# Kernel tuning notes

Hardware: AMD Instinct MI355X
Metric: run time of the kernel (lower is better)

Reference implementation:

```python
import jax, jax.numpy as jnp
import numpy as np

N_QUBITS = 10
N_QLAYERS = 2
EMBED = 1024
B, S = 16, 1024
DIM = 2 ** N_QUBITS


def _apply_rx(state, theta, w, n):
    # state: [N, 2^n] complex; RX(theta) on wire w (wire 0 = most significant bit)
    nb = state.shape[0]
    left, right = 2 ** w, 2 ** (n - 1 - w)
    psi = state.reshape(nb, left, 2, right)
    t = jnp.asarray(theta, jnp.float32) * 0.5
    c, s = jnp.cos(t), jnp.sin(t)
    if c.ndim == 1:  # per-sample angles
        c, s = c[:, None, None], s[:, None, None]
    a0, a1 = psi[:, :, 0, :], psi[:, :, 1, :]
    n0 = c * a0 - 1j * s * a1
    n1 = -1j * s * a0 + c * a1
    return jnp.stack([n0, n1], axis=2).reshape(nb, -1)


def _apply_cnot(state, c, t, n):
    # CNOT with control wire c, target wire t
    psi = state.reshape((-1,) + (2,) * n)
    ctrl_ax, tgt_ax = c + 1, t + 1
    psi0, psi1 = jnp.split(psi, 2, axis=ctrl_ax)
    psi1 = jnp.flip(psi1, axis=tgt_ax)
    return jnp.concatenate([psi0, psi1], axis=ctrl_ax).reshape(state.shape)


def setup_inputs() -> dict:
    key = jax.random.key(0)
    ks = jax.random.split(key, 6)
    s1 = 1.0 / np.sqrt(EMBED)
    s2 = 1.0 / np.sqrt(N_QUBITS)
    return {
        "x": jax.random.normal(ks[0], (B, S, EMBED), jnp.float32),
        "W1": jax.random.uniform(ks[1], (N_QUBITS, EMBED), jnp.float32, -s1, s1),
        "b1": jax.random.uniform(ks[2], (N_QUBITS,), jnp.float32, -s1, s1),
        "qweights": jax.random.uniform(ks[3], (N_QLAYERS, N_QUBITS), jnp.float32, 0.0, 2.0 * np.pi),
        "W2": jax.random.uniform(ks[4], (EMBED, N_QUBITS), jnp.float32, -s2, s2),
        "b2": jax.random.uniform(ks[5], (EMBED,), jnp.float32, -s2, s2),
    }


def reference(x, W1, b1, qweights, W2, b2):
    n = N_QUBITS
    # linear_1
    ang = (jnp.einsum('bse,qe->bsq', x, W1) + b1).reshape(-1, n)  # [N, n]
    N = ang.shape[0]
    # |0...0> batched state vector
    state = jnp.zeros((N, DIM), jnp.complex64).at[:, 0].set(1.0)
    # AngleEmbedding: RX(ang[:, w]) on each wire
    for w in range(n):
        state = _apply_rx(state, ang[:, w], w, n)
    # BasicEntanglerLayers: RX rotations + CNOT ring per layer
    for l in range(N_QLAYERS):
        for w in range(n):
            state = _apply_rx(state, qweights[l, w], w, n)
        if n == 2:
            state = _apply_cnot(state, 0, 1, n)
        elif n > 2:
            for i in range(n):
                state = _apply_cnot(state, i, (i + 1) % n, n)
    # <Z_w> = sum_idx probs[idx] * (1 - 2*bit_w(idx))
    probs = jnp.real(state * jnp.conj(state))  # [N, 2^n]
    idx = jnp.arange(DIM)
    bits = (idx[:, None] >> (n - 1 - jnp.arange(n))[None, :]) & 1
    signs = (1 - 2 * bits).astype(jnp.float32)  # [2^n, n]
    ev = (probs @ signs).reshape(x.shape[0], x.shape[1], n)  # [B, S, n]
    # linear_2
    return jnp.einsum('bsq,eq->bse', ev, W2) + b2
```

## Files before the change

### kernel.cpp

```cpp
#include <hip/hip_runtime.h>

#define NQ 10
#define EMBED 1024
#define ROWS_PER_BLOCK 32
#define BLOCK 512


constexpr int kPop(int x) { int c = 0; for (int i = 0; i < 10; ++i) c += (x >> i) & 1; return c; }

constexpr int sigma_map(int a) {
    int b = 0;
    for (int i = 0; i < 9; ++i) b |= (((a >> i) & 1) ^ ((a >> (i + 1)) & 1)) << i;
    b |= (((a >> 9) & 1) ^ ((a >> 0) & 1) ^ ((a >> 1) & 1)) << 9;
    return b;
}

#define MAXT 40
struct Terms {
    int nt[NQ];
    int vm[NQ];
    int um[NQ];
    unsigned short tm[NQ][MAXT];
    unsigned short sm[NQ][MAXT];
    float sg[NQ][MAXT];
};

constexpr Terms gen_terms() {
    Terms t{};
    int inv_e[NQ] = {};
    for (int a = 0; a < 1024; ++a) {
        const int s = sigma_map(a);
        for (int q = 0; q < NQ; ++q) if (s == (1 << q)) inv_e[q] = a;
    }
    for (int q = 0; q < NQ; ++q) {
        const int u = inv_e[q];
        int v = 0;
        for (int w = 0; w < NQ; ++w) if ((u >> w) & 1) v ^= inv_e[w];
        t.um[q] = u; t.vm[q] = v;
        int n = 0;
        int S = 0;
        while (true) {
            int T = (((S >> 0) ^ (S >> 9)) & 1)
                  | ((((S >> 0) ^ (S >> 1) ^ (S >> 9)) & 1) << 1);
            for (int j = 2; j < 10; ++j) T |= ((((S >> (j - 1)) ^ (S >> j)) & 1) << j);
            if ((T & ~v) == 0) {
                const int p = kPop(T) + kPop(S);
                if (!(p & 1)) {
                    t.tm[q][n] = (unsigned short)T;
                    t.sm[q][n] = (unsigned short)S;
                    t.sg[q][n] = (p & 2) ? -1.f : 1.f;
                    ++n;
                }
            }
            if (S == u) break;
            S = (S - u) & u;
        }
        t.nt[q] = n;
    }
    return t;
}

constexpr Terms TT = gen_terms();

template <int CTRL, int RM>
__device__ __forceinline__ float dppadd(float v) {
    const int s = __builtin_amdgcn_update_dpp(0, __float_as_int(v), CTRL, RM, 0xF, true);
    return v + __int_as_float(s);
}
__device__ __forceinline__ float red32(float v) {
    v = dppadd<0xB1,  0xF>(v);
    v = dppadd<0x4E,  0xF>(v);
    v = dppadd<0x141, 0xF>(v);
    v = dppadd<0x140, 0xF>(v);
    v = dppadd<0x142, 0xA>(v);
    return v;
}

#define FMA1(ACC, XV, WW)                 \
    ACC = fmaf((XV).x, (WW).x, ACC);      \
    ACC = fmaf((XV).y, (WW).y, ACC);      \
    ACC = fmaf((XV).z, (WW).z, ACC);      \
    ACC = fmaf((XV).w, (WW).w, ACC);

extern "C" __global__ __launch_bounds__(BLOCK, 4)
void ffq_kernel(const float* __restrict__ x, const float* __restrict__ W1,
                const float* __restrict__ b1, const float* __restrict__ qw,
                const float* __restrict__ W2, const float* __restrict__ b2,
                float* __restrict__ out)
{
    __shared__ float sW1[NQ * EMBED];
    __shared__ float sCA[ROWS_PER_BLOCK][11];
    __shared__ float sSA[ROWS_PER_BLOCK][11];
    __shared__ float sEVv[ROWS_PER_BLOCK][11];

    const int tid  = threadIdx.x;
    const int lane = tid & 63;
    const int wv   = tid >> 6;
    const int o    = lane & 31;
    const int g    = lane >> 5;
    const int block0 = blockIdx.x * ROWS_PER_BLOCK;

    {
        const float4* src = (const float4*)W1;
        float4* dst = (float4*)sW1;
        #pragma unroll
        for (int i = 0; i < 5; ++i) dst[tid + BLOCK * i] = src[tid + BLOCK * i];
    }
    __syncthreads();

    {
        const int rloc0 = wv * 4 + g * 2;
        const float4* xr0 = (const float4*)(x + (size_t)(block0 + rloc0) * EMBED);
        const float4* xr1 = (const float4*)(x + (size_t)(block0 + rloc0 + 1) * EMBED);
        const float4* w1v = (const float4*)sW1;

        float4 xv0[4], xv1[4];
        #pragma unroll
        for (int k = 0; k < 4; ++k) { xv0[k] = xr0[k * 32 + o]; xv1[k] = xr1[k * 32 + o]; }

        float acc0[NQ], acc1[NQ];
        #pragma unroll
        for (int q = 0; q < NQ; ++q) { acc0[q] = 0.f; acc1[q] = 0.f; }

        float4 wA[5], wB[5], wC[5];

        #define HLOAD(BUF, H) {                                                  \
            _Pragma("unroll")                                                    \
            for (int q = 0; q < 5; ++q)                                          \
                BUF[q] = w1v[(((H) & 1) * 5 + q) * 256 + ((H) >> 1) * 32 + o];   \
        }
        #define HFMA(BUF, H) {                                                   \
            _Pragma("unroll")                                                    \
            for (int q = 0; q < 5; ++q) {                                        \
                FMA1(acc0[((H) & 1) * 5 + q], xv0[((H) >> 1) & 3], BUF[q]);      \
                FMA1(acc1[((H) & 1) * 5 + q], xv1[((H) >> 1) & 3], BUF[q]);      \
            }                                                                    \
        }
        #define XREFILL(K) {                                                     \
            xv0[(K) & 3] = xr0[((K) + 4) * 32 + o];                              \
            xv1[(K) & 3] = xr1[((K) + 4) * 32 + o];                              \
        }

        HLOAD(wA, 0);
        HLOAD(wB, 1);
        HLOAD(wC, 2);  HFMA(wA, 0);
        HLOAD(wA, 3);  HFMA(wB, 1);  XREFILL(0);
        HLOAD(wB, 4);  HFMA(wC, 2);
        HLOAD(wC, 5);  HFMA(wA, 3);  XREFILL(1);
        HLOAD(wA, 6);  HFMA(wB, 4);
        HLOAD(wB, 7);  HFMA(wC, 5);  XREFILL(2);
        HLOAD(wC, 8);  HFMA(wA, 6);
        HLOAD(wA, 9);  HFMA(wB, 7);  XREFILL(3);
        HLOAD(wB, 10); HFMA(wC, 8);
        HLOAD(wC, 11); HFMA(wA, 9);
        HLOAD(wA, 12); HFMA(wB, 10);
        HLOAD(wB, 13); HFMA(wC, 11);
        HLOAD(wC, 14); HFMA(wA, 12);
        HLOAD(wA, 15); HFMA(wB, 13);
                       HFMA(wC, 14);
                       HFMA(wA, 15);
        #undef HLOAD
        #undef HFMA
        #undef XREFILL

        #pragma unroll
        for (int q = 0; q < NQ; ++q) {
            acc0[q] = red32(acc0[q]);
            acc1[q] = red32(acc1[q]);
        }

        if (o == 16) {
            #pragma unroll
            for (int w = 0; w < NQ; ++w) {
                const float A = acc0[w] + b1[w] + qw[w];
                sCA[rloc0][w] = __cosf(A);
                sSA[rloc0][w] = __sinf(A);
            }
        } else if (o == 17) {
            #pragma unroll
            for (int w = 0; w < NQ; ++w) {
                const float A = acc1[w] + b1[w] + qw[w];
                sCA[rloc0 + 1][w] = __cosf(A);
                sSA[rloc0 + 1][w] = __sinf(A);
            }
        }
    }

    const int e4 = tid & 255;
    float w2f[40];
    {
        const float4* w2v = (const float4*)(W2 + e4 * 40);
        #pragma unroll
        for (int i = 0; i < 10; ++i) {
            float4 v = w2v[i];
            w2f[4*i+0] = v.x; w2f[4*i+1] = v.y; w2f[4*i+2] = v.z; w2f[4*i+3] = v.w;
        }
    }
    const float4 b2v = ((const float4*)b2)[e4];

    __syncthreads();

    if (lane < ROWS_PER_BLOCK) {
        const int row = lane;
        float ca[NQ], sa[NQ], cb[NQ], sb[NQ];
        #pragma unroll
        for (int w = 0; w < NQ; ++w) {
            ca[w] = sCA[row][w];
            sa[w] = sSA[row][w];
            const float B = qw[NQ + w];
            cb[w] = __cosf(B); sb[w] = __sinf(B);
        }
        #define EVQ(QC) do {                                                      \
            float ev = 0.f;                                                       \
            _Pragma("unroll")                                                     \
            for (int k = 0; k < TT.nt[QC]; ++k) {                                 \
                float P = TT.sg[QC][k];                                           \
                _Pragma("unroll")                                                 \
                for (int w = 0; w < NQ; ++w) {                                    \
                    if ((TT.vm[QC] >> w) & 1) P *= ((TT.tm[QC][k] >> w) & 1) ? sa[w] : ca[w]; \
                    if ((TT.um[QC] >> w) & 1) P *= ((TT.sm[QC][k] >> w) & 1) ? sb[w] : cb[w]; \
                }                                                                 \
                ev += P;                                                          \
            }                                                                     \
            sEVv[row][QC] = ev;                                                   \
        } while (0)
        switch (wv) {
            case 0: EVQ(0); break;
            case 1: EVQ(9); break;
            case 2: EVQ(7); break;
            case 3: EVQ(8); break;
            case 4: EVQ(5); EVQ(6); break;
            case 5: EVQ(3); EVQ(4); break;
            case 6: EVQ(1); EVQ(2); break;
            default: break;
        }
        #undef EVQ
    }

    __syncthreads();

    const int r0 = (tid >> 8) * 16;
    #pragma unroll
    for (int r = 0; r < 16; ++r) {
        const int rr = r0 + r;
        float evr[NQ];
        #pragma unroll
        for (int q = 0; q < NQ; ++q) evr[q] = sEVv[rr][q];
        float o0 = b2v.x, o1 = b2v.y, o2 = b2v.z, o3 = b2v.w;
        #pragma unroll
        for (int q = 0; q < NQ; ++q) {
            o0 = fmaf(evr[q], w2f[ 0 + q], o0);
            o1 = fmaf(evr[q], w2f[10 + q], o1);
            o2 = fmaf(evr[q], w2f[20 + q], o2);
            o3 = fmaf(evr[q], w2f[30 + q], o3);
        }
        float4 ov = {o0, o1, o2, o3};
        ((float4*)(out + (size_t)(block0 + rr) * EMBED))[e4] = ov;
    }
}

extern "C" void kernel_launch(void* const* d_in, const int* in_sizes, int n_in,
                              void* d_out, int out_size, void* d_ws, size_t ws_size,
                              hipStream_t stream) {
    (void)in_sizes; (void)n_in; (void)d_ws; (void)ws_size; (void)out_size;
    const float* x  = (const float*)d_in[0];
    const float* W1 = (const float*)d_in[1];
    const float* b1 = (const float*)d_in[2];
    const float* qw = (const float*)d_in[3];
    const float* W2 = (const float*)d_in[4];
    const float* b2 = (const float*)d_in[5];
    float* out = (float*)d_out;

    const int total_rows = 16 * 1024;
    dim3 grid(total_rows / ROWS_PER_BLOCK);
    ffq_kernel<<<grid, BLOCK, 0, stream>>>(x, W1, b1, qw, W2, b2, out);
}
```

Before: 28.35 us.

## Split fused kernel into expectation-value kernel and output projection kernel

Splits the single fused kernel into two launches. The first computes the per-row quantum expectation values and stashes them in the first ten floats of each output row. The second reads them back and runs the linear_2 projection on smaller 256-thread blocks of 8 rows each. The intent is to decouple the register-heavy expectation phase from the store-bound output phase and give the write stage more parallelism, at the cost of an extra launch and an extra global round trip for the expectation values.

New measurement: 36.06 us. 27.2% more time.

```diff
diff --git a/kernel.cpp b/kernel.cpp
--- a/kernel.cpp
+++ b/kernel.cpp
@@ -83,15 +83,13 @@
     ACC = fmaf((XV).w, (WW).w, ACC);
 
 extern "C" __global__ __launch_bounds__(BLOCK, 4)
-void ffq_kernel(const float* __restrict__ x, const float* __restrict__ W1,
-                const float* __restrict__ b1, const float* __restrict__ qw,
-                const float* __restrict__ W2, const float* __restrict__ b2,
-                float* __restrict__ out)
+void ffq_ev_kernel(const float* __restrict__ x, const float* __restrict__ W1,
+                   const float* __restrict__ b1, const float* __restrict__ qw,
+                   float* __restrict__ out)
 {
     __shared__ float sW1[NQ * EMBED];
     __shared__ float sCA[ROWS_PER_BLOCK][11];
     __shared__ float sSA[ROWS_PER_BLOCK][11];
-    __shared__ float sEVv[ROWS_PER_BLOCK][11];
 
     const int tid  = threadIdx.x;
     const int lane = tid & 63;
@@ -186,18 +184,6 @@
         }
     }
 
-    const int e4 = tid & 255;
-    float w2f[40];
-    {
-        const float4* w2v = (const float4*)(W2 + e4 * 40);
-        #pragma unroll
-        for (int i = 0; i < 10; ++i) {
-            float4 v = w2v[i];
-            w2f[4*i+0] = v.x; w2f[4*i+1] = v.y; w2f[4*i+2] = v.z; w2f[4*i+3] = v.w;
-        }
-    }
-    const float4 b2v = ((const float4*)b2)[e4];
-
     __syncthreads();
 
     if (lane < ROWS_PER_BLOCK) {
@@ -210,6 +196,7 @@
             const float B = qw[NQ + w];
             cb[w] = __cosf(B); sb[w] = __sinf(B);
         }
+        float* orow = out + (size_t)(block0 + row) * EMBED;
         #define EVQ(QC) do {                                                      \
             float ev = 0.f;                                                       \
             _Pragma("unroll")                                                     \
@@ -222,7 +209,7 @@
                 }                                                                 \
                 ev += P;                                                          \
             }                                                                     \
-            sEVv[row][QC] = ev;                                                   \
+            orow[QC] = ev;                                                        \
         } while (0)
         switch (wv) {
             case 0: EVQ(0); break;
@@ -236,26 +223,48 @@
         }
         #undef EVQ
     }
-
+}
+
+extern "C" __global__ __launch_bounds__(256, 4)
+void ffq_out_kernel(const float* __restrict__ W2, const float* __restrict__ b2,
+                    float* __restrict__ out)
+{
+    __shared__ float sev[80];
+
+    const int tid = threadIdx.x;
+    const int r0  = blockIdx.x * 8;
+
+    float w2f[40];
+    {
+        const float4* w2v = (const float4*)(W2 + tid * 40);
+        #pragma unroll
+        for (int i = 0; i < 10; ++i) {
+            float4 v = w2v[i];
+            w2f[4*i+0] = v.x; w2f[4*i+1] = v.y; w2f[4*i+2] = v.z; w2f[4*i+3] = v.w;
+        }
+    }
+    const float4 b2v = ((const float4*)b2)[tid];
+
+    if (tid < 80) {
+        const int rr = tid / 10;
+        const int qq = tid - rr * 10;
+        sev[tid] = out[(size_t)(r0 + rr) * EMBED + qq];
+    }
     __syncthreads();
 
-    const int r0 = (tid >> 8) * 16;
     #pragma unroll
-    for (int r = 0; r < 16; ++r) {
-        const int rr = r0 + r;
-        float evr[NQ];
-        #pragma unroll
-        for (int q = 0; q < NQ; ++q) evr[q] = sEVv[rr][q];
+    for (int rr = 0; rr < 8; ++rr) {
         float o0 = b2v.x, o1 = b2v.y, o2 = b2v.z, o3 = b2v.w;
         #pragma unroll
         for (int q = 0; q < NQ; ++q) {
-            o0 = fmaf(evr[q], w2f[ 0 + q], o0);
-            o1 = fmaf(evr[q], w2f[10 + q], o1);
-            o2 = fmaf(evr[q], w2f[20 + q], o2);
-            o3 = fmaf(evr[q], w2f[30 + q], o3);
+            const float e = sev[rr * 10 + q];
+            o0 = fmaf(e, w2f[ 0 + q], o0);
+            o1 = fmaf(e, w2f[10 + q], o1);
+            o2 = fmaf(e, w2f[20 + q], o2);
+            o3 = fmaf(e, w2f[30 + q], o3);
         }
         float4 ov = {o0, o1, o2, o3};
-        ((float4*)(out + (size_t)(block0 + rr) * EMBED))[e4] = ov;
+        ((float4*)(out + (size_t)(r0 + rr) * EMBED))[tid] = ov;
     }
 }
 
@@ -271,7 +280,6 @@
     const float* b2 = (const float*)d_in[5];
     float* out = (float*)d_out;
 
-    const int total_rows = 16 * 1024;
-    dim3 grid(total_rows / ROWS_PER_BLOCK);
-    ffq_kernel<<<grid, BLOCK, 0, stream>>>(x, W1, b1, qw, W2, b2, out);
-}
+    ffq_ev_kernel<<<dim3(512), BLOCK, 0, stream>>>(x, W1, b1, qw, out);
+    ffq_out_kernel<<<dim3(2048), 256, 0, stream>>>(W2, b2, out);
+}
```
